# Optimization experiments

Hardware: AMD Instinct MI355X
Metric: run time of the kernel (lower is better)

The kernel has to match this reference:

```python
import jax, jax.numpy as jnp
import numpy as np

B, T, D, H = 8, 1024, 1024, 16
HD = D // H  # 64
FF = 4 * D


def setup_inputs() -> dict:
    key = jax.random.key(0)
    ks = jax.random.split(key, 16)
    s = lambda k, shape, scale: (jax.random.normal(k, shape, dtype=jnp.float32) * scale)
    return {
        "x": s(ks[0], (B, T, D), 1.0),
        "ln1_g": jnp.ones((D,), jnp.float32),
        "ln1_b": jnp.zeros((D,), jnp.float32),
        "ln2_g": jnp.ones((D,), jnp.float32),
        "ln2_b": jnp.zeros((D,), jnp.float32),
        "Wq": s(ks[1], (H, D, HD), 0.02), "bq": jnp.zeros((H, HD), jnp.float32),
        "Wk": s(ks[2], (H, D, HD), 0.02), "bk": jnp.zeros((H, HD), jnp.float32),
        "Wv": s(ks[3], (H, D, HD), 0.02), "bv": jnp.zeros((H, HD), jnp.float32),
        "Wo": s(ks[4], (D, D), 0.02), "bo": jnp.zeros((D,), jnp.float32),
        "W1": s(ks[5], (D, FF), 0.02), "b1": jnp.zeros((FF,), jnp.float32),
        "W2": s(ks[6], (FF, D), 0.02), "b2": jnp.zeros((D,), jnp.float32),
    }


def layer_norm(x, g, b, eps=1e-5):
    mu = jnp.mean(x, axis=-1, keepdims=True)
    var = jnp.mean(jnp.square(x - mu), axis=-1, keepdims=True)
    return (x - mu) * jax.lax.rsqrt(var + eps) * g + b


def reference(x, ln1_g, ln1_b, ln2_g, ln2_b, Wq, bq, Wk, bk, Wv, bv, Wo, bo, W1, b1, W2, b2):
    h = layer_norm(x, ln1_g, ln1_b)
    # Per-head Q/K/V projections, batched over heads (equivalent to the
    # Python loop of per-head Linears in the original module).
    q = jnp.einsum("btd,hde->bhte", h, Wq) + bq[None, :, None, :]
    k = jnp.einsum("btd,hde->bhte", h, Wk) + bk[None, :, None, :]
    v = jnp.einsum("btd,hde->bhte", h, Wv) + bv[None, :, None, :]
    scores = jnp.einsum("bhte,bhse->bhts", q, k) / jnp.sqrt(jnp.float32(HD))
    att = jax.nn.softmax(scores, axis=-1)  # no causal mask in source
    ctx = jnp.einsum("bhts,bhse->bhte", att, v)
    # concat heads along feature dim
    ctx = jnp.transpose(ctx, (0, 2, 1, 3)).reshape(B, T, D)
    attn_out = ctx @ Wo + bo
    x = x + attn_out
    h2 = layer_norm(x, ln2_g, ln2_b)
    ff = jax.nn.gelu(h2 @ W1 + b1, approximate=False) @ W2 + b2
    return x + ff
```

## Files before the change

kernel.cpp:

```cpp
#include <hip/hip_runtime.h>
#include <hip/hip_bf16.h>
#include <cstdint>
#include <cstddef>


typedef __bf16 bf16;
typedef __bf16 bf16x8 __attribute__((ext_vector_type(8)));
typedef __bf16 bf16x4 __attribute__((ext_vector_type(4)));
typedef float  f32x4  __attribute__((ext_vector_type(4)));

#define BB    8
#define TT    1024
#define DD    1024
#define HH    16
#define HDIM  64
#define FFD   4096
#define MROWS (BB*TT)

__device__ __forceinline__ void async_ld16(const void* g, void* l) {
  __builtin_amdgcn_global_load_lds(
      (const __attribute__((address_space(1))) uint32_t*)g,
      (__attribute__((address_space(3))) uint32_t*)l, 16, 0, 0);
}

__global__ void k_transpose_cast(const float* __restrict__ src, bf16* __restrict__ dst,
                                 int K, int N) {
  __shared__ float tile[32][33];
  const size_t boff = (size_t)blockIdx.z * K * N;
  src += boff; dst += boff;
  const int k0 = blockIdx.y * 32, n0 = blockIdx.x * 32;
  const int tx = threadIdx.x, ty = threadIdx.y;
#pragma unroll
  for (int i = 0; i < 4; ++i)
    tile[ty + i*8][tx] = src[(size_t)(k0 + ty + i*8) * N + n0 + tx];
  __syncthreads();
#pragma unroll
  for (int i = 0; i < 4; ++i)
    dst[(size_t)(n0 + ty + i*8) * K + k0 + tx] = (bf16)tile[tx][ty + i*8];
}

__global__ void k_concat_bias(const float* __restrict__ bq, const float* __restrict__ bk,
                              const float* __restrict__ bv, float* __restrict__ out) {
  int i = blockIdx.x * 256 + threadIdx.x;
  float v = (i < 1024) ? bq[i] : (i < 2048) ? bk[i - 1024] : bv[i - 2048];
  out[i] = v;
}

__global__ void k_transpose_v(const bf16* __restrict__ qkv, bf16* __restrict__ vT) {
  __shared__ bf16 tile[32][33];
  const int bh = blockIdx.z;
  const int b = bh >> 4, h = bh & 15;
  const int t0 = blockIdx.x * 32, e0 = blockIdx.y * 32;
  const int tx = threadIdx.x, ty = threadIdx.y;
  const bf16* src = qkv + (size_t)b * TT * 3072 + 2048 + h * 64;
#pragma unroll
  for (int i = 0; i < 4; ++i)
    tile[ty + i*8][tx] = src[(size_t)(t0 + ty + i*8) * 3072 + e0 + tx];
  __syncthreads();
  bf16* dst = vT + ((size_t)bh * 64 + e0) * TT + t0;
#pragma unroll
  for (int i = 0; i < 4; ++i)
    dst[(size_t)(ty + i*8) * TT + tx] = tile[tx][ty + i*8];
}

__global__ void k_layernorm(const float* __restrict__ x, const float* __restrict__ g,
                            const float* __restrict__ b, bf16* __restrict__ out) {
  const int row = blockIdx.x, tid = threadIdx.x;
  const float* xr = x + (size_t)row * DD;
  f32x4 v = *(const f32x4*)(xr + tid * 4);
  float s  = v[0] + v[1] + v[2] + v[3];
  float ss = v[0]*v[0] + v[1]*v[1] + v[2]*v[2] + v[3]*v[3];
#pragma unroll
  for (int m = 1; m < 64; m <<= 1) { s += __shfl_xor(s, m); ss += __shfl_xor(ss, m); }
  __shared__ float red[8];
  const int wid = tid >> 6;
  if ((tid & 63) == 0) { red[wid*2] = s; red[wid*2+1] = ss; }
  __syncthreads();
  s  = red[0] + red[2] + red[4] + red[6];
  ss = red[1] + red[3] + red[5] + red[7];
  const float mu = s * (1.0f / DD);
  const float var = ss * (1.0f / DD) - mu * mu;
  const float rs = rsqrtf(var + 1e-5f);
  bf16x4 o;
#pragma unroll
  for (int j = 0; j < 4; ++j)
    o[j] = (bf16)((v[j] - mu) * rs * g[tid*4 + j] + b[tid*4 + j]);
  *(bf16x4*)&out[(size_t)row * DD + tid * 4] = o;
}

template<int MODE>
__global__ __launch_bounds__(512, 2)
void k_gemm256(const bf16* __restrict__ A, const bf16* __restrict__ Bt,
               const float* __restrict__ bias, bf16* __restrict__ outb,
               int M, int N, int K) {
  __shared__ __align__(16) bf16 As[2][256 * 64];
  __shared__ __align__(16) bf16 Bs[2][256 * 64];
  const int tid = threadIdx.x;
  const int w = tid >> 6, l = tid & 63;
  const int wm = w >> 2, wn = w & 3;
  const int l15 = l & 15, l4 = l >> 4;

  const int nbx = N >> 8;
  const int nwg = gridDim.x;
  const int cpx = nwg >> 3;
  const int swz = (blockIdx.x & 7) * cpx + (blockIdx.x >> 3);
  const int m0 = (swz / nbx) << 8, n0 = (swz % nbx) << 8;

  f32x4 acc[8][4] = {};

  const int srow = l >> 3;
  const int sch = l & 7;

  const int NT = K >> 6;

#define STAGE_A(buf, kt, rb) { \
    const int r_ = (rb) + w*8 + srow; \
    const int ch_ = sch ^ (r_ & 7); \
    async_ld16(A + (size_t)(m0 + r_) * K + (kt)*64 + ch_*8, &As[buf][((rb) + w*8)*64]); }
#define STAGE_B(buf, kt, rb) { \
    const int r_ = (rb) + w*8 + srow; \
    const int ch_ = sch ^ (r_ & 7); \
    async_ld16(Bt + (size_t)(n0 + r_) * K + (kt)*64 + ch_*8, &Bs[buf][((rb) + w*8)*64]); }

  STAGE_A(0, 0, 0)   STAGE_A(0, 0, 64)  STAGE_A(0, 0, 128) STAGE_A(0, 0, 192)
  STAGE_B(0, 0, 0)   STAGE_B(0, 0, 64)  STAGE_B(0, 0, 128) STAGE_B(0, 0, 192)
  STAGE_A(1, 1, 0)   STAGE_A(1, 1, 64)  STAGE_A(1, 1, 128) STAGE_A(1, 1, 192)
  asm volatile("s_waitcnt vmcnt(4)" ::: "memory");
  __builtin_amdgcn_sched_barrier(0);
  __builtin_amdgcn_s_barrier();

  for (int t = 0; t < NT; ++t) {
    const int p = t & 1;
    bf16x8 b0[4], b1[4], af[4], ag[4];

#pragma unroll
    for (int nf = 0; nf < 4; ++nf) {
      const int row = wn*64 + nf*16 + l15;
      b0[nf] = *(const bf16x8*)&Bs[p][row*64 + (l4 ^ (row & 7))*8];
    }
#pragma unroll
    for (int mf = 0; mf < 4; ++mf) {
      const int row = wm*128 + mf*16 + l15;
      af[mf] = *(const bf16x8*)&As[p][row*64 + (l4 ^ (row & 7))*8];
    }
    if (t + 1 < NT) { STAGE_B(p^1, t+1, 0) STAGE_B(p^1, t+1, 64) }
    __builtin_amdgcn_s_barrier();
    asm volatile("s_waitcnt lgkmcnt(0)" ::: "memory");
    __builtin_amdgcn_sched_barrier(0);
    __builtin_amdgcn_s_setprio(1);
#pragma unroll
    for (int mf = 0; mf < 4; ++mf)
#pragma unroll
      for (int nf = 0; nf < 4; ++nf)
        acc[mf][nf] = __builtin_amdgcn_mfma_f32_16x16x32_bf16(af[mf], b0[nf], acc[mf][nf], 0, 0, 0);
    __builtin_amdgcn_s_setprio(0);
    __builtin_amdgcn_s_barrier();

#pragma unroll
    for (int mf = 0; mf < 4; ++mf) {
      const int row = wm*128 + (mf+4)*16 + l15;
      ag[mf] = *(const bf16x8*)&As[p][row*64 + (l4 ^ (row & 7))*8];
    }
    if (t + 1 < NT) { STAGE_B(p^1, t+1, 128) STAGE_B(p^1, t+1, 192) }
    __builtin_amdgcn_s_barrier();
    asm volatile("s_waitcnt lgkmcnt(0)" ::: "memory");
    __builtin_amdgcn_sched_barrier(0);
    __builtin_amdgcn_s_setprio(1);
#pragma unroll
    for (int mf = 0; mf < 4; ++mf)
#pragma unroll
      for (int nf = 0; nf < 4; ++nf)
        acc[mf+4][nf] = __builtin_amdgcn_mfma_f32_16x16x32_bf16(ag[mf], b0[nf], acc[mf+4][nf], 0, 0, 0);
    __builtin_amdgcn_s_setprio(0);
    __builtin_amdgcn_s_barrier();

#pragma unroll
    for (int nf = 0; nf < 4; ++nf) {
      const int row = wn*64 + nf*16 + l15;
      b1[nf] = *(const bf16x8*)&Bs[p][row*64 + ((4+l4) ^ (row & 7))*8];
    }
#pragma unroll
    for (int mf = 0; mf < 4; ++mf) {
      const int row = wm*128 + mf*16 + l15;
      af[mf] = *(const bf16x8*)&As[p][row*64 + ((4+l4) ^ (row & 7))*8];
    }
#pragma unroll
    for (int mf = 0; mf < 4; ++mf) {
      const int row = wm*128 + (mf+4)*16 + l15;
      ag[mf] = *(const bf16x8*)&As[p][row*64 + ((4+l4) ^ (row & 7))*8];
    }
    __builtin_amdgcn_s_barrier();
    asm volatile("s_waitcnt lgkmcnt(0)" ::: "memory");
    __builtin_amdgcn_sched_barrier(0);
    __builtin_amdgcn_s_setprio(1);
#pragma unroll
    for (int mf = 0; mf < 4; ++mf)
#pragma unroll
      for (int nf = 0; nf < 4; ++nf)
        acc[mf][nf] = __builtin_amdgcn_mfma_f32_16x16x32_bf16(af[mf], b1[nf], acc[mf][nf], 0, 0, 0);
    __builtin_amdgcn_s_setprio(0);
    __builtin_amdgcn_s_barrier();

    if (t + 2 < NT) { STAGE_A(p, t+2, 0) STAGE_A(p, t+2, 64)
                      STAGE_A(p, t+2, 128) STAGE_A(p, t+2, 192) }
    __builtin_amdgcn_s_setprio(1);
#pragma unroll
    for (int mf = 0; mf < 4; ++mf)
#pragma unroll
      for (int nf = 0; nf < 4; ++nf)
        acc[mf+4][nf] = __builtin_amdgcn_mfma_f32_16x16x32_bf16(ag[mf], b1[nf], acc[mf+4][nf], 0, 0, 0);
    __builtin_amdgcn_s_setprio(0);
    if (t < NT - 2) { asm volatile("s_waitcnt vmcnt(4)" ::: "memory"); }
    else            { asm volatile("s_waitcnt vmcnt(0)" ::: "memory"); }
    __builtin_amdgcn_sched_barrier(0);
    __builtin_amdgcn_s_barrier();
  }
#undef STAGE_A
#undef STAGE_B

#pragma unroll
  for (int mf = 0; mf < 8; ++mf) {
#pragma unroll
    for (int r = 0; r < 4; ++r) {
      const size_t grow = (size_t)(m0 + wm*128 + mf*16 + l4*4 + r);
      const size_t rowoff = grow * (size_t)N;
#pragma unroll
      for (int nf = 0; nf < 4; ++nf) {
        const int gcol = n0 + wn*64 + nf*16 + l15;
        float v = acc[mf][nf][r] + bias[gcol];
        if constexpr (MODE == 1)
          v = 0.5f * v * (1.0f + erff(v * 0.70710678118654752440f));
        outb[rowoff + gcol] = (bf16)v;
      }
    }
  }
}

template<int MODE>
__global__ __launch_bounds__(256)
void k_gemm(const bf16* __restrict__ A, const bf16* __restrict__ Bt,
            const float* __restrict__ bias, const float* __restrict__ res,
            bf16* __restrict__ outb, float* __restrict__ outf,
            int M, int N, int K) {
  __shared__ __align__(16) bf16 As[128 * 64];
  __shared__ __align__(16) bf16 Bs[128 * 64];
  const int tid = threadIdx.x;
  const int w = tid >> 6, l = tid & 63;
  const int wm = w >> 1, wn = w & 1;
  const int l15 = l & 15, l4 = l >> 4;
  const int m0 = blockIdx.y * 128, n0 = blockIdx.x * 128;

  f32x4 acc[4][4] = {};

  const int srow0 = w * 32 + (l >> 3);
  const int sl7 = l & 7;

  for (int k0 = 0; k0 < K; k0 += 64) {
#pragma unroll
    for (int j = 0; j < 4; ++j) {
      const int row = srow0 + j * 8;
      const int ch = sl7 ^ (row & 7);
      async_ld16(A + (size_t)(m0 + row) * K + k0 + ch * 8, &As[(w*32 + j*8) * 64]);
    }
#pragma unroll
    for (int j = 0; j < 4; ++j) {
      const int row = srow0 + j * 8;
      const int ch = sl7 ^ (row & 7);
      async_ld16(Bt + (size_t)(n0 + row) * K + k0 + ch * 8, &Bs[(w*32 + j*8) * 64]);
    }
    __syncthreads();
#pragma unroll
    for (int kk = 0; kk < 2; ++kk) {
      bf16x8 af[4], bfr[4];
#pragma unroll
      for (int mf = 0; mf < 4; ++mf) {
        const int row = wm*64 + mf*16 + l15;
        const int ch = (kk*4 + l4) ^ (row & 7);
        af[mf] = *(const bf16x8*)&As[row*64 + ch*8];
      }
#pragma unroll
      for (int nf = 0; nf < 4; ++nf) {
        const int row = wn*64 + nf*16 + l15;
        const int ch = (kk*4 + l4) ^ (row & 7);
        bfr[nf] = *(const bf16x8*)&Bs[row*64 + ch*8];
      }
#pragma unroll
      for (int mf = 0; mf < 4; ++mf)
#pragma unroll
        for (int nf = 0; nf < 4; ++nf)
          acc[mf][nf] = __builtin_amdgcn_mfma_f32_16x16x32_bf16(af[mf], bfr[nf], acc[mf][nf], 0, 0, 0);
    }
    __syncthreads();
  }

#pragma unroll
  for (int mf = 0; mf < 4; ++mf) {
#pragma unroll
    for (int r = 0; r < 4; ++r) {
      const size_t grow = (size_t)(m0 + wm*64 + mf*16 + l4*4 + r);
      const size_t rowoff = grow * (size_t)N;
#pragma unroll
      for (int nf = 0; nf < 4; ++nf) {
        const int gcol = n0 + wn*64 + nf*16 + l15;
        float v = acc[mf][nf][r] + bias[gcol];
        if constexpr (MODE == 1)
          v = 0.5f * v * (1.0f + erff(v * 0.70710678118654752440f));
        if constexpr (MODE == 2) {
          v += res[rowoff + gcol];
          outf[rowoff + gcol] = v;
        } else {
          outb[rowoff + gcol] = (bf16)v;
        }
      }
    }
  }
}

__global__ __launch_bounds__(512)
void k_attn(const bf16* __restrict__ qkv, const bf16* __restrict__ vT,
            bf16* __restrict__ ctx) {
  const int tid = threadIdx.x;
  const int w = tid >> 6, l = tid & 63;
  const int l15 = l & 15, l4 = l >> 4;

  const int gid = ((int)blockIdx.x & 7) * 128 + ((int)blockIdx.x >> 3);
  const int qt = gid & 7;
  const int bh = gid >> 3;
  const int h = bh & 15, b = bh >> 4;

  __shared__ __align__(16) bf16 Ks[2][64 * 64];
  __shared__ __align__(16) bf16 Vs[2][64 * 64];
  __shared__ __align__(16) bf16 P[8][16][72];

  const bf16* base = qkv + (size_t)b * TT * 3072;
  const bf16* Qp = base + h * 64;
  const bf16* Kp = base + 1024 + h * 64;
  const bf16* Vtp = vT + (size_t)bh * HDIM * TT;

  const int qrow = qt * 128 + w * 16 + l15;
  bf16x8 qf[2];
  qf[0] = *(const bf16x8*)&Qp[(size_t)qrow * 3072 + l4 * 8];
  qf[1] = *(const bf16x8*)&Qp[(size_t)qrow * 3072 + 32 + l4 * 8];

  f32x4 oacc[4] = {};
  float mrow[4] = {-1e30f, -1e30f, -1e30f, -1e30f};
  float lrow[4] = {0.f, 0.f, 0.f, 0.f};

  const int srow = w * 8 + (l >> 3);
  const int sch = (l & 7) ^ (srow & 7);

  auto stage = [&](int buf, int t) {
    const int kv0 = t * 64;
    async_ld16(Kp + (size_t)(kv0 + srow) * 3072 + sch * 8, &Ks[buf][w * 512]);
    async_ld16(Vtp + (size_t)srow * TT + kv0 + sch * 8, &Vs[buf][w * 512]);
  };

  stage(0, 0);
  for (int t = 0; t < TT / 64; ++t) {
    const int cur = t & 1;
    __syncthreads();
    if (t + 1 < TT / 64) stage(cur ^ 1, t + 1);

    f32x4 sacc[4] = {};
#pragma unroll
    for (int nf = 0; nf < 4; ++nf) {
      const int row = nf*16 + l15;
#pragma unroll
      for (int kk = 0; kk < 2; ++kk) {
        const int ch = (kk*4 + l4) ^ (row & 7);
        bf16x8 kfr = *(const bf16x8*)&Ks[cur][row*64 + ch*8];
        sacc[nf] = __builtin_amdgcn_mfma_f32_16x16x32_bf16(qf[kk], kfr, sacc[nf], 0, 0, 0);
      }
    }
    float mx[4];
    int ok = 1;
#pragma unroll
    for (int r = 0; r < 4; ++r) {
      float m = -1e30f;
#pragma unroll
      for (int nf = 0; nf < 4; ++nf) { sacc[nf][r] *= 0.125f; m = fmaxf(m, sacc[nf][r]); }
      m = fmaxf(m, __shfl_xor(m, 1));
      m = fmaxf(m, __shfl_xor(m, 2));
      m = fmaxf(m, __shfl_xor(m, 4));
      m = fmaxf(m, __shfl_xor(m, 8));
      mx[r] = m;
      ok &= (m <= mrow[r] + 8.0f);
    }
    if (!__all(ok)) {
#pragma unroll
      for (int r = 0; r < 4; ++r) {
        const float mn = fmaxf(mrow[r], mx[r]);
        const float e = __expf(mrow[r] - mn);
        mrow[r] = mn;
        lrow[r] *= e;
#pragma unroll
        for (int nf = 0; nf < 4; ++nf) oacc[nf][r] *= e;
      }
    }
#pragma unroll
    for (int r = 0; r < 4; ++r) {
      float rs = 0.f;
#pragma unroll
      for (int nf = 0; nf < 4; ++nf) {
        const float pv = __expf(sacc[nf][r] - mrow[r]);
        rs += pv;
        P[w][l4*4 + r][l15 + nf*16] = (bf16)pv;
      }
      rs += __shfl_xor(rs, 1); rs += __shfl_xor(rs, 2);
      rs += __shfl_xor(rs, 4); rs += __shfl_xor(rs, 8);
      lrow[r] += rs;
    }
#pragma unroll
    for (int kk = 0; kk < 2; ++kk) {
      bf16x8 pa = *(const bf16x8*)&P[w][l15][kk*32 + l4*8];
#pragma unroll
      for (int nf = 0; nf < 4; ++nf) {
        const int row = nf*16 + l15;
        const int ch = (kk*4 + l4) ^ (row & 7);
        bf16x8 vb = *(const bf16x8*)&Vs[cur][row*64 + ch*8];
        oacc[nf] = __builtin_amdgcn_mfma_f32_16x16x32_bf16(pa, vb, oacc[nf], 0, 0, 0);
      }
    }
  }
  bf16* outp = ctx + ((size_t)b * TT + qt * 128 + w * 16) * DD + h * 64;
#pragma unroll
  for (int nf = 0; nf < 4; ++nf)
#pragma unroll
    for (int r = 0; r < 4; ++r)
      outp[(size_t)(l4*4 + r) * DD + l15 + nf*16] = (bf16)(oacc[nf][r] / lrow[r]);
}

extern "C" void kernel_launch(void* const* d_in, const int* in_sizes, int n_in,
                              void* d_out, int out_size, void* d_ws, size_t ws_size,
                              hipStream_t stream) {
  const float* x     = (const float*)d_in[0];
  const float* ln1_g = (const float*)d_in[1];
  const float* ln1_b = (const float*)d_in[2];
  const float* ln2_g = (const float*)d_in[3];
  const float* ln2_b = (const float*)d_in[4];
  const float* Wq    = (const float*)d_in[5];
  const float* bq    = (const float*)d_in[6];
  const float* Wk    = (const float*)d_in[7];
  const float* bk    = (const float*)d_in[8];
  const float* Wv    = (const float*)d_in[9];
  const float* bv    = (const float*)d_in[10];
  const float* Wo    = (const float*)d_in[11];
  const float* bo    = (const float*)d_in[12];
  const float* W1    = (const float*)d_in[13];
  const float* b1    = (const float*)d_in[14];
  const float* W2    = (const float*)d_in[15];
  const float* b2    = (const float*)d_in[16];
  float* out = (float*)d_out;

  char* ws = (char*)d_ws;
  bf16* h1    = (bf16*)(ws + 0);
  bf16* vT    = (bf16*)(ws + 0);
  bf16* qkv   = (bf16*)(ws + 16777216);
  bf16* ctx   = (bf16*)(ws + 67108864);
  bf16* u     = (bf16*)(ws + 16777216);
  float* x1   = (float*)(ws + 83886080);
  bf16* wtqkv = (bf16*)(ws + 117440512);
  bf16* wot   = (bf16*)(ws + 123731968);
  bf16* w1t   = (bf16*)(ws + 125829120);
  bf16* w2t   = (bf16*)(ws + 134217728);
  float* bqkv = (float*)(ws + 142606336);
  bf16* h2 = h1;

  dim3 tb(32, 8);
  k_transpose_cast<<<dim3(2, 32, 16), tb, 0, stream>>>(Wq, wtqkv, DD, HDIM);
  k_transpose_cast<<<dim3(2, 32, 16), tb, 0, stream>>>(Wk, wtqkv + 1024*1024, DD, HDIM);
  k_transpose_cast<<<dim3(2, 32, 16), tb, 0, stream>>>(Wv, wtqkv + 2048*1024, DD, HDIM);
  k_transpose_cast<<<dim3(32, 32, 1), tb, 0, stream>>>(Wo, wot, DD, DD);
  k_transpose_cast<<<dim3(128, 32, 1), tb, 0, stream>>>(W1, w1t, DD, FFD);
  k_transpose_cast<<<dim3(32, 128, 1), tb, 0, stream>>>(W2, w2t, FFD, DD);
  k_concat_bias<<<dim3(12), 256, 0, stream>>>(bq, bk, bv, bqkv);

  k_layernorm<<<dim3(MROWS), 256, 0, stream>>>(x, ln1_g, ln1_b, h1);

  k_gemm256<0><<<dim3((MROWS/256)*(3072/256)), 512, 0, stream>>>(
      h1, wtqkv, bqkv, qkv, MROWS, 3072, DD);

  k_transpose_v<<<dim3(32, 2, 128), tb, 0, stream>>>(qkv, vT);

  k_attn<<<dim3(1024), 512, 0, stream>>>(qkv, vT, ctx);

  k_gemm<2><<<dim3(8, 64), 256, 0, stream>>>(ctx, wot, bo, x,
                                             nullptr, x1, MROWS, DD, DD);

  k_layernorm<<<dim3(MROWS), 256, 0, stream>>>(x1, ln2_g, ln2_b, h2);

  k_gemm256<1><<<dim3((MROWS/256)*(FFD/256)), 512, 0, stream>>>(
      h2, w1t, b1, u, MROWS, FFD, DD);

  k_gemm<2><<<dim3(8, 64), 256, 0, stream>>>(u, w2t, b2, x1,
                                             nullptr, out, MROWS, DD, FFD);

  (void)in_sizes; (void)n_in; (void)out_size; (void)ws_size;
}
```

Baseline: 443.8 us.

## Precompute LDS/global addresses, unroll GEMM loop by two, use tanh GELU

The 256-tile GEMM main loop is unrolled by two so the double-buffer indices become compile-time constants. The swizzled LDS read and global staging pointers are precomputed once instead of recomputing row/XOR addresses every iteration, and the 128-tile GEMM gets the same address hoisting. The exact erf GELU in the epilogue is replaced by a tanh approximation built on fast exp and divide. That approximation differs from the reference's exact GELU and may cost accuracy.

```diff
diff --git a/kernel.cpp b/kernel.cpp
--- a/kernel.cpp
+++ b/kernel.cpp
@@ -21,6 +21,14 @@
   __builtin_amdgcn_global_load_lds(
       (const __attribute__((address_space(1))) uint32_t*)g,
       (__attribute__((address_space(3))) uint32_t*)l, 16, 0, 0);
+}
+
+__device__ __forceinline__ float gelu_f(float v) {
+  float z = 0.7978845608028654f * (v + 0.044715f * v * v * v);
+  z = fminf(fmaxf(z, -9.0f), 9.0f);
+  const float e = __expf(-2.0f * z);
+  const float th = 1.0f - __fdividef(2.0f * e, 1.0f + e);
+  return 0.5f * v * (1.0f + th);
 }
 
 __global__ void k_transpose_cast(const float* __restrict__ src, bf16* __restrict__ dst,
@@ -108,115 +116,113 @@
 
   f32x4 acc[8][4] = {};
 
-  const int srow = l >> 3;
-  const int sch = l & 7;
+  const int l7 = l15 & 7;
+  const int c0 = (l4 ^ l7) * 8;
+  const int c1 = ((4 + l4) ^ l7) * 8;
+  const bf16* const A00 = &As[0][(wm*128 + l15)*64 + c0];
+  const bf16* const A01 = &As[0][(wm*128 + l15)*64 + c1];
+  const bf16* const A10 = &As[1][(wm*128 + l15)*64 + c0];
+  const bf16* const A11 = &As[1][(wm*128 + l15)*64 + c1];
+  const bf16* const B00 = &Bs[0][(wn*64 + l15)*64 + c0];
+  const bf16* const B01 = &Bs[0][(wn*64 + l15)*64 + c1];
+  const bf16* const B10 = &Bs[1][(wn*64 + l15)*64 + c0];
+  const bf16* const B11 = &Bs[1][(wn*64 + l15)*64 + c1];
+
+  const int srow = l >> 3, sch = l & 7;
+  const int schx = (sch ^ srow) * 8;
+  const bf16* const aG0 = A  + (size_t)(m0 + w*8 + srow) * K + schx;
+  const bf16* const aG1 = aG0 + (size_t)64 * K;
+  const bf16* const aG2 = aG0 + (size_t)128 * K;
+  const bf16* const aG3 = aG0 + (size_t)192 * K;
+  const bf16* const bG0 = Bt + (size_t)(n0 + w*8 + srow) * K + schx;
+  const bf16* const bG1 = bG0 + (size_t)64 * K;
+  const bf16* const bG2 = bG0 + (size_t)128 * K;
+  const bf16* const bG3 = bG0 + (size_t)192 * K;
+  bf16* const LA0 = (bf16*)As[0] + w*512;
+  bf16* const LA1 = (bf16*)As[1] + w*512;
+  bf16* const LB0 = (bf16*)Bs[0] + w*512;
+  bf16* const LB1 = (bf16*)Bs[1] + w*512;
 
   const int NT = K >> 6;
 
-#define STAGE_A(buf, kt, rb) { \
-    const int r_ = (rb) + w*8 + srow; \
-    const int ch_ = sch ^ (r_ & 7); \
-    async_ld16(A + (size_t)(m0 + r_) * K + (kt)*64 + ch_*8, &As[buf][((rb) + w*8)*64]); }
-#define STAGE_B(buf, kt, rb) { \
-    const int r_ = (rb) + w*8 + srow; \
-    const int ch_ = sch ^ (r_ & 7); \
-    async_ld16(Bt + (size_t)(n0 + r_) * K + (kt)*64 + ch_*8, &Bs[buf][((rb) + w*8)*64]); }
-
-  STAGE_A(0, 0, 0)   STAGE_A(0, 0, 64)  STAGE_A(0, 0, 128) STAGE_A(0, 0, 192)
-  STAGE_B(0, 0, 0)   STAGE_B(0, 0, 64)  STAGE_B(0, 0, 128) STAGE_B(0, 0, 192)
-  STAGE_A(1, 1, 0)   STAGE_A(1, 1, 64)  STAGE_A(1, 1, 128) STAGE_A(1, 1, 192)
+#define RD_B(reg, base) { _Pragma("unroll") \
+    for (int nf = 0; nf < 4; ++nf) reg[nf] = *(const bf16x8*)((base) + nf*1024); }
+#define RD_A(reg, base, mb) { _Pragma("unroll") \
+    for (int mf = 0; mf < 4; ++mf) reg[mf] = *(const bf16x8*)((base) + (mb+mf)*1024); }
+#define MM(areg, breg, mb) { _Pragma("unroll") \
+    for (int mf = 0; mf < 4; ++mf) _Pragma("unroll") \
+      for (int nf = 0; nf < 4; ++nf) \
+        acc[mb+mf][nf] = __builtin_amdgcn_mfma_f32_16x16x32_bf16(areg[mf], breg[nf], acc[mb+mf][nf], 0, 0, 0); }
+#define SGA(off, lb) { async_ld16(aG0 + (off), (lb)+0*64);  async_ld16(aG1 + (off), (lb)+64*64); \
+                       async_ld16(aG2 + (off), (lb)+128*64); async_ld16(aG3 + (off), (lb)+192*64); }
+#define SGB2a(off, lb) { async_ld16(bG0 + (off), (lb)+0*64);   async_ld16(bG1 + (off), (lb)+64*64); }
+#define SGB2b(off, lb) { async_ld16(bG2 + (off), (lb)+128*64); async_ld16(bG3 + (off), (lb)+192*64); }
+#define WAIT_LGKM { asm volatile("s_waitcnt lgkmcnt(0)" ::: "memory"); __builtin_amdgcn_sched_barrier(0); }
+#define BAR __builtin_amdgcn_s_barrier()
+
+  SGA(0, LA0)  SGB2a(0, LB0) SGB2b(0, LB0)  SGA(64, LA1)
   asm volatile("s_waitcnt vmcnt(4)" ::: "memory");
   __builtin_amdgcn_sched_barrier(0);
-  __builtin_amdgcn_s_barrier();
-
-  for (int t = 0; t < NT; ++t) {
-    const int p = t & 1;
-    bf16x8 b0[4], b1[4], af[4], ag[4];
-
-#pragma unroll
-    for (int nf = 0; nf < 4; ++nf) {
-      const int row = wn*64 + nf*16 + l15;
-      b0[nf] = *(const bf16x8*)&Bs[p][row*64 + (l4 ^ (row & 7))*8];
-    }
-#pragma unroll
-    for (int mf = 0; mf < 4; ++mf) {
-      const int row = wm*128 + mf*16 + l15;
-      af[mf] = *(const bf16x8*)&As[p][row*64 + (l4 ^ (row & 7))*8];
-    }
-    if (t + 1 < NT) { STAGE_B(p^1, t+1, 0) STAGE_B(p^1, t+1, 64) }
-    __builtin_amdgcn_s_barrier();
-    asm volatile("s_waitcnt lgkmcnt(0)" ::: "memory");
+  BAR;
+
+  size_t ko = 0;
+  for (int T = 0; T < NT; T += 2) {
+    const bool nl  = (T + 2 < NT);
+    const bool nl2 = (T + 3 < NT);
+    bf16x8 b0[4], b1[4], alo[4], ahi[4];
+
+    RD_B(b0, B00) RD_A(alo, A00, 0)
+    SGB2a(ko + 64, LB1)
+    BAR; WAIT_LGKM;
+    __builtin_amdgcn_s_setprio(1); MM(alo, b0, 0) __builtin_amdgcn_s_setprio(0);
+    BAR;
+    RD_A(ahi, A00, 4)
+    SGB2b(ko + 64, LB1)
+    BAR; WAIT_LGKM;
+    __builtin_amdgcn_s_setprio(1); MM(ahi, b0, 4) __builtin_amdgcn_s_setprio(0);
+    BAR;
+    RD_B(b1, B01) RD_A(alo, A01, 0) RD_A(ahi, A01, 4)
+    BAR; WAIT_LGKM;
+    __builtin_amdgcn_s_setprio(1); MM(alo, b1, 0) __builtin_amdgcn_s_setprio(0);
+    BAR;
+    if (nl) SGA(ko + 128, LA0)
+    __builtin_amdgcn_s_setprio(1); MM(ahi, b1, 4) __builtin_amdgcn_s_setprio(0);
+    if (nl) { asm volatile("s_waitcnt vmcnt(4)" ::: "memory"); }
+    else    { asm volatile("s_waitcnt vmcnt(0)" ::: "memory"); }
     __builtin_amdgcn_sched_barrier(0);
-    __builtin_amdgcn_s_setprio(1);
-#pragma unroll
-    for (int mf = 0; mf < 4; ++mf)
-#pragma unroll
-      for (int nf = 0; nf < 4; ++nf)
-        acc[mf][nf] = __builtin_amdgcn_mfma_f32_16x16x32_bf16(af[mf], b0[nf], acc[mf][nf], 0, 0, 0);
-    __builtin_amdgcn_s_setprio(0);
-    __builtin_amdgcn_s_barrier();
-
-#pragma unroll
-    for (int mf = 0; mf < 4; ++mf) {
-      const int row = wm*128 + (mf+4)*16 + l15;
-      ag[mf] = *(const bf16x8*)&As[p][row*64 + (l4 ^ (row & 7))*8];
-    }
-    if (t + 1 < NT) { STAGE_B(p^1, t+1, 128) STAGE_B(p^1, t+1, 192) }
-    __builtin_amdgcn_s_barrier();
-    asm volatile("s_waitcnt lgkmcnt(0)" ::: "memory");
+    BAR;
+
+    RD_B(b0, B10) RD_A(alo, A10, 0)
+    if (nl) SGB2a(ko + 128, LB0)
+    BAR; WAIT_LGKM;
+    __builtin_amdgcn_s_setprio(1); MM(alo, b0, 0) __builtin_amdgcn_s_setprio(0);
+    BAR;
+    RD_A(ahi, A10, 4)
+    if (nl) SGB2b(ko + 128, LB0)
+    BAR; WAIT_LGKM;
+    __builtin_amdgcn_s_setprio(1); MM(ahi, b0, 4) __builtin_amdgcn_s_setprio(0);
+    BAR;
+    RD_B(b1, B11) RD_A(alo, A11, 0) RD_A(ahi, A11, 4)
+    BAR; WAIT_LGKM;
+    __builtin_amdgcn_s_setprio(1); MM(alo, b1, 0) __builtin_amdgcn_s_setprio(0);
+    BAR;
+    if (nl2) SGA(ko + 192, LA1)
+    __builtin_amdgcn_s_setprio(1); MM(ahi, b1, 4) __builtin_amdgcn_s_setprio(0);
+    if (nl2) { asm volatile("s_waitcnt vmcnt(4)" ::: "memory"); }
+    else     { asm volatile("s_waitcnt vmcnt(0)" ::: "memory"); }
     __builtin_amdgcn_sched_barrier(0);
-    __builtin_amdgcn_s_setprio(1);
-#pragma unroll
-    for (int mf = 0; mf < 4; ++mf)
-#pragma unroll
-      for (int nf = 0; nf < 4; ++nf)
-        acc[mf+4][nf] = __builtin_amdgcn_mfma_f32_16x16x32_bf16(ag[mf], b0[nf], acc[mf+4][nf], 0, 0, 0);
-    __builtin_amdgcn_s_setprio(0);
-    __builtin_amdgcn_s_barrier();
-
-#pragma unroll
-    for (int nf = 0; nf < 4; ++nf) {
-      const int row = wn*64 + nf*16 + l15;
-      b1[nf] = *(const bf16x8*)&Bs[p][row*64 + ((4+l4) ^ (row & 7))*8];
-    }
-#pragma unroll
-    for (int mf = 0; mf < 4; ++mf) {
-      const int row = wm*128 + mf*16 + l15;
-      af[mf] = *(const bf16x8*)&As[p][row*64 + ((4+l4) ^ (row & 7))*8];
-    }
-#pragma unroll
-    for (int mf = 0; mf < 4; ++mf) {
-      const int row = wm*128 + (mf+4)*16 + l15;
-      ag[mf] = *(const bf16x8*)&As[p][row*64 + ((4+l4) ^ (row & 7))*8];
-    }
-    __builtin_amdgcn_s_barrier();
-    asm volatile("s_waitcnt lgkmcnt(0)" ::: "memory");
-    __builtin_amdgcn_sched_barrier(0);
-    __builtin_amdgcn_s_setprio(1);
-#pragma unroll
-    for (int mf = 0; mf < 4; ++mf)
-#pragma unroll
-      for (int nf = 0; nf < 4; ++nf)
-        acc[mf][nf] = __builtin_amdgcn_mfma_f32_16x16x32_bf16(af[mf], b1[nf], acc[mf][nf], 0, 0, 0);
-    __builtin_amdgcn_s_setprio(0);
-    __builtin_amdgcn_s_barrier();
-
-    if (t + 2 < NT) { STAGE_A(p, t+2, 0) STAGE_A(p, t+2, 64)
-                      STAGE_A(p, t+2, 128) STAGE_A(p, t+2, 192) }
-    __builtin_amdgcn_s_setprio(1);
-#pragma unroll
-    for (int mf = 0; mf < 4; ++mf)
-#pragma unroll
-      for (int nf = 0; nf < 4; ++nf)
-        acc[mf+4][nf] = __builtin_amdgcn_mfma_f32_16x16x32_bf16(ag[mf], b1[nf], acc[mf+4][nf], 0, 0, 0);
-    __builtin_amdgcn_s_setprio(0);
-    if (t < NT - 2) { asm volatile("s_waitcnt vmcnt(4)" ::: "memory"); }
-    else            { asm volatile("s_waitcnt vmcnt(0)" ::: "memory"); }
-    __builtin_amdgcn_sched_barrier(0);
-    __builtin_amdgcn_s_barrier();
+    BAR;
+
+    ko += 128;
   }
-#undef STAGE_A
-#undef STAGE_B
+#undef RD_B
+#undef RD_A
+#undef MM
+#undef SGA
+#undef SGB2a
+#undef SGB2b
+#undef WAIT_LGKM
+#undef BAR
 
 #pragma unroll
   for (int mf = 0; mf < 8; ++mf) {
@@ -228,8 +234,7 @@
       for (int nf = 0; nf < 4; ++nf) {
         const int gcol = n0 + wn*64 + nf*16 + l15;
         float v = acc[mf][nf][r] + bias[gcol];
-        if constexpr (MODE == 1)
-          v = 0.5f * v * (1.0f + erff(v * 0.70710678118654752440f));
+        if constexpr (MODE == 1) v = gelu_f(v);
         outb[rowoff + gcol] = (bf16)v;
       }
     }
@@ -252,38 +257,38 @@
 
   f32x4 acc[4][4] = {};
 
-  const int srow0 = w * 32 + (l >> 3);
-  const int sl7 = l & 7;
+  const int l7 = l15 & 7;
+  const int c0 = (l4 ^ l7) * 8, c1 = ((4 + l4) ^ l7) * 8;
+  const bf16* const Ab = &As[(wm*64 + l15)*64];
+  const bf16* const Bb = &Bs[(wn*64 + l15)*64];
+
+  const int sr8 = l >> 3, sl7 = l & 7;
+  const int schx = (sl7 ^ sr8) * 8;
+  const bf16* const gA0 = A  + (size_t)(m0 + w*32 + sr8) * K + schx;
+  const bf16* const gA1 = gA0 + (size_t)8 * K;
+  const bf16* const gA2 = gA0 + (size_t)16 * K;
+  const bf16* const gA3 = gA0 + (size_t)24 * K;
+  const bf16* const gB0 = Bt + (size_t)(n0 + w*32 + sr8) * K + schx;
+  const bf16* const gB1 = gB0 + (size_t)8 * K;
+  const bf16* const gB2 = gB0 + (size_t)16 * K;
+  const bf16* const gB3 = gB0 + (size_t)24 * K;
+  bf16* const lA = (bf16*)As + w*32*64;
+  bf16* const lB = (bf16*)Bs + w*32*64;
 
   for (int k0 = 0; k0 < K; k0 += 64) {
-#pragma unroll
-    for (int j = 0; j < 4; ++j) {
-      const int row = srow0 + j * 8;
-      const int ch = sl7 ^ (row & 7);
-      async_ld16(A + (size_t)(m0 + row) * K + k0 + ch * 8, &As[(w*32 + j*8) * 64]);
-    }
-#pragma unroll
-    for (int j = 0; j < 4; ++j) {
-      const int row = srow0 + j * 8;
-      const int ch = sl7 ^ (row & 7);
-      async_ld16(Bt + (size_t)(n0 + row) * K + k0 + ch * 8, &Bs[(w*32 + j*8) * 64]);
-    }
+    async_ld16(gA0 + k0, lA);          async_ld16(gA1 + k0, lA + 8*64);
+    async_ld16(gA2 + k0, lA + 16*64);  async_ld16(gA3 + k0, lA + 24*64);
+    async_ld16(gB0 + k0, lB);          async_ld16(gB1 + k0, lB + 8*64);
+    async_ld16(gB2 + k0, lB + 16*64);  async_ld16(gB3 + k0, lB + 24*64);
     __syncthreads();
 #pragma unroll
     for (int kk = 0; kk < 2; ++kk) {
+      const int cc = kk ? c1 : c0;
       bf16x8 af[4], bfr[4];
 #pragma unroll
-      for (int mf = 0; mf < 4; ++mf) {
-        const int row = wm*64 + mf*16 + l15;
-        const int ch = (kk*4 + l4) ^ (row & 7);
-        af[mf] = *(const bf16x8*)&As[row*64 + ch*8];
-      }
-#pragma unroll
-      for (int nf = 0; nf < 4; ++nf) {
-        const int row = wn*64 + nf*16 + l15;
-        const int ch = (kk*4 + l4) ^ (row & 7);
-        bfr[nf] = *(const bf16x8*)&Bs[row*64 + ch*8];
-      }
+      for (int mf = 0; mf < 4; ++mf) af[mf] = *(const bf16x8*)(Ab + mf*1024 + cc);
+#pragma unroll
+      for (int nf = 0; nf < 4; ++nf) bfr[nf] = *(const bf16x8*)(Bb + nf*1024 + cc);
 #pragma unroll
       for (int mf = 0; mf < 4; ++mf)
 #pragma unroll
@@ -303,8 +308,7 @@
       for (int nf = 0; nf < 4; ++nf) {
         const int gcol = n0 + wn*64 + nf*16 + l15;
         float v = acc[mf][nf][r] + bias[gcol];
-        if constexpr (MODE == 1)
-          v = 0.5f * v * (1.0f + erff(v * 0.70710678118654752440f));
+        if constexpr (MODE == 1) v = gelu_f(v);
         if constexpr (MODE == 2) {
           v += res[rowoff + gcol];
           outf[rowoff + gcol] = v;
```

Result: no change. 444.4 us (+0.1%).
